# Kernel optimization log

Measured on AMD Instinct MI355X. Metric: run time of the kernel, lower is better.

Reference implementation:

```python
import jax, jax.numpy as jnp
import numpy as np

SUB_NO = 20
T_NO = 200
NB = 19            # cos_basis_no
COS_SHIFT = 1.0
COS_SCALE = 5.0
T_DATA = 100000
E_NO = 2000
I_NO = 400


def _cos_basis():
    x = jnp.arange(T_NO, dtype=jnp.float32)
    raw = COS_SCALE * jnp.log(x + COS_SHIFT)                      # [T_no]
    phi = (jnp.pi / 2.0) * jnp.arange(NB, dtype=jnp.float32)[:, None]  # [NB,1]
    basis = 0.5 * jnp.cos(raw[None, :] - phi) + 0.5               # [NB, T_no]
    mask = (raw[None, :] >= phi - jnp.pi) & (raw[None, :] <= phi + jnp.pi)
    return jnp.where(mask, basis, 0.0)


def _gconv(x, kern_flipped):
    # depthwise (grouped) 1d cross-correlation, VALID padding, matching torch F.conv1d
    # x: [L, sub], kern_flipped: [sub, T_no] (already time-flipped) -> [L - T_no + 1, sub]
    out = jax.lax.conv_general_dilated(
        x.T[None],                      # [1, sub, L]
        kern_flipped[:, None, :],       # [sub, 1, T_no]
        window_strides=(1,), padding='VALID',
        feature_group_count=x.shape[1],
        dimension_numbers=('NCH', 'OIH', 'NCH'))
    return out[0].T


def setup_inputs() -> dict:
    key = jax.random.key(0)
    ks = jax.random.split(key, 16)
    rng = np.random.default_rng(0)
    # tree adjacency: each node j>0 has a parent < j; C_den[parent, child] = 1
    C_den = np.zeros((SUB_NO, SUB_NO), np.float32)
    for j in range(1, SUB_NO):
        C_den[rng.integers(0, j), j] = 1.0
    # one-hot synapse -> subunit maps
    C_syn_e = np.zeros((SUB_NO, E_NO), np.float32)
    C_syn_e[rng.integers(0, SUB_NO, E_NO), np.arange(E_NO)] = 1.0
    C_syn_i = np.zeros((SUB_NO, I_NO), np.float32)
    C_syn_i[rng.integers(0, SUB_NO, I_NO), np.arange(I_NO)] = 1.0
    # sparse binary spike trains
    S_e = (jax.random.uniform(ks[0], (T_DATA, E_NO)) < 0.02).astype(jnp.float32)
    S_i = (jax.random.uniform(ks[1], (T_DATA, I_NO)) < 0.02).astype(jnp.float32)
    Z = (jax.random.uniform(ks[2], (T_DATA, SUB_NO)) < 0.05).astype(jnp.float32)
    return {
        'S_e': S_e, 'S_i': S_i, 'Z': Z,
        'C_den': jnp.asarray(C_den), 'C_syn_e': jnp.asarray(C_syn_e), 'C_syn_i': jnp.asarray(C_syn_i),
        'W_syn': 0.1 * jax.random.normal(ks[3], (SUB_NO, NB, 2)),
        'W_hist': 0.1 * jax.random.normal(ks[4], (SUB_NO, NB)),
        'W_spk': jnp.ones(SUB_NO) + 0.05 * jax.random.normal(ks[5], (SUB_NO,)),
        'Delta_spk': jax.random.uniform(ks[6], (SUB_NO,), maxval=2.0),
        'Tau_spk': 3.0 * jnp.ones(SUB_NO) + 0.1 * jax.random.normal(ks[7], (SUB_NO,)),
        'V_o': jax.random.normal(ks[8], (1,)),
        'Theta': 0.1 * jax.random.normal(ks[9], (SUB_NO,)),
        'weight1': 0.1 * jax.random.normal(ks[10], (SUB_NO, 6)),
        'weight2': 0.1 * jax.random.normal(ks[11], (6, 6)),
        'weight3': 0.1 * jax.random.normal(ks[12], (6, SUB_NO)),
    }


def reference(S_e, S_i, Z, C_den, C_syn_e, C_syn_i, W_syn, W_hist, W_spk,
              Delta_spk, Tau_spk, V_o, Theta, weight1, weight2, weight3):
    cb = _cos_basis()                                  # [NB, T_no]
    sub = C_den.shape[0]
    pad = lambda x, n: jnp.concatenate([jnp.zeros((n, sub), x.dtype), x], axis=0)

    # --- spike_convolve ---
    syn_e = S_e @ C_syn_e.T                            # [T, sub]
    syn_i = S_i @ C_syn_i.T
    e_kern = W_syn[:, :, 0] @ cb                       # [sub, T_no]
    i_kern = W_syn[:, :, 1] @ cb
    filtered_e = _gconv(pad(syn_e, T_NO - 1), jnp.flip(e_kern, 1))
    filtered_i = _gconv(pad(syn_i, T_NO - 1), jnp.flip(i_kern, 1))
    syn = filtered_e + filtered_i                      # [T, sub]

    # --- history and spike kernels (causal, 1-step delayed: pad T_no, drop last) ---
    hist_kern = W_hist @ cb                            # [sub, T_no]
    pad_Z = pad(Z, T_NO)                               # [T + T_no, sub]
    hist_filt = _gconv(pad_Z, jnp.flip(hist_kern, 1))[:-1]   # [T, sub]

    t = jnp.maximum(jnp.arange(T_NO, dtype=jnp.float32)[None, :] - Delta_spk[:, None], 0.0)
    t_tau = t / (Tau_spk[:, None] ** 2)
    spk_kern = t_tau * jnp.exp(-t_tau) * (W_spk[:, None] ** 2)  # [sub, T_no]
    spk_filt = _gconv(pad_Z, jnp.flip(spk_kern, 1))[:-1]        # [T, sub]

    # --- per-subunit loop, vectorized: leaf gather == spk_filt @ C_den.T ---
    sub_in = syn + Theta[None, :] + hist_filt + spk_filt @ C_den.T   # [T, sub]
    h0 = jax.nn.leaky_relu(sub_in)
    h1 = jax.nn.leaky_relu(h0[:, :, None] * weight1[None, :, :])     # [T, sub, 6]
    h2 = jax.nn.leaky_relu(jnp.einsum('tsk,kj->tsj', h1, weight2))   # [T, sub, 6]
    final_Z = jax.nn.sigmoid(jnp.einsum('tsj,js->ts', h2, weight3))  # [T, sub]

    final_V = spk_filt[:, 0] + V_o[0]                  # [T]
    out_filters = jnp.concatenate([e_kern, i_kern, hist_kern, spk_kern], axis=0)  # [4*sub, T_no]
    return final_V, final_Z, out_filters
```

## Files before the change

### kernel.cpp

```cpp
#include <hip/hip_runtime.h>

typedef unsigned short ushort_t;
typedef unsigned int uint_t;

#define T_DATA 100000
#define E_NO 2000
#define I_NO 400
#define SUB 20
#define TNO 200
#define NBASIS 19
#define HEAD 256
#define TAILPAD 2048
#define SIGSTRIDE (HEAD + T_DATA + TAILPAD)
#define TILE 2048
#define RPT 8

#define OFF_Z  ((size_t)T_DATA)
#define OFF_F  ((size_t)T_DATA + (size_t)T_DATA*SUB)

__device__ __forceinline__ float b2f(ushort_t u) {
    union { uint_t i; float f; } v; v.i = ((uint_t)u) << 16; return v.f;
}
__device__ __forceinline__ ushort_t f2b(float f) {
    union { uint_t i; float f_; } v; v.f_ = f;
    uint_t b = v.i;
    uint_t r = (b + 0x7FFFu + ((b >> 16) & 1u)) >> 16;
    return (ushort_t)r;
}
__device__ __forceinline__ float ldin(const void* p, size_t idx, int mode) {
    return mode ? b2f(((const ushort_t*)p)[idx]) : ((const float*)p)[idx];
}
__device__ __forceinline__ void stout(void* p, size_t idx, float val, int mode) {
    if (mode) ((ushort_t*)p)[idx] = f2b(val);
    else      ((float*)p)[idx] = val;
}
__device__ __forceinline__ float f4get(const float4& v, int i) {
    return i == 0 ? v.x : i == 1 ? v.y : i == 2 ? v.z : v.w;
}
__device__ __forceinline__ float pick12(const float4& L, const float4& M, const float4& H, int e) {
    return e < 4 ? f4get(L, e) : e < 8 ? f4get(M, e - 4) : f4get(H, e - 8);
}

__global__ void k_probe(const void* tau, int* flag) {
    if (threadIdx.x == 0) {
        const ushort_t* tu = (const ushort_t*)tau;
        int cnt = 0;
        for (int i = 0; i < 20; ++i) {
            float v = b2f(tu[i]);
            if (v >= 1.5f && v < 6.0f) cnt++;
        }
        *flag = (cnt >= 15) ? 1 : 0;
    }
}

__global__ __launch_bounds__(256) void k0_prep(
        const int* __restrict__ flag,
        const void* Csyn_e, const void* Csyn_i,
        const void* W_syn, const void* W_hist,
        const void* W_spk, const void* Delta, const void* Tau,
        float* ws_f, int* mape, int* mapi, ushort_t* sigs, void* dout) {
    int mode = *flag;
    int bid = blockIdx.x, tid = threadIdx.x;
    if (bid < 80) {
        int kidx = bid / 20, s = bid % 20;
        int tau = tid;
        if (tau < TNO) {
            float val;
            if (kidx < 3) {
                float raw = 5.0f * logf((float)tau + 1.0f);
                val = 0.f;
                for (int b = 0; b < NBASIS; ++b) {
                    float phi = 1.5707963267948966f * (float)b;
                    float d = raw - phi;
                    float basis = (d >= -3.14159265358979f && d <= 3.14159265358979f)
                                  ? (0.5f * cosf(d) + 0.5f) : 0.f;
                    float w = (kidx == 0) ? ldin(W_syn, (size_t)s * NBASIS * 2 + b * 2 + 0, mode)
                            : (kidx == 1) ? ldin(W_syn, (size_t)s * NBASIS * 2 + b * 2 + 1, mode)
                                          : ldin(W_hist, (size_t)s * NBASIS + b, mode);
                    val += w * basis;
                }
            } else {
                float dl = ldin(Delta, s, mode), tu = ldin(Tau, s, mode), wk = ldin(W_spk, s, mode);
                float t = fmaxf((float)tau - dl, 0.f);
                float tt = t / (tu * tu);
                val = tt * expf(-tt) * (wk * wk);
            }
            ws_f[kidx * 4000 + s * TNO + tau] = val;
            stout(dout, OFF_F + (size_t)bid * TNO + tau, val, mode);
        }
    } else if (bid < 96) {
        int e = (bid - 80) * 256 + tid;
        if (e < E_NO) {
            int m = 0;
            for (int s = 0; s < SUB; ++s)
                if (ldin(Csyn_e, (size_t)s * E_NO + e, mode) != 0.f) { m = s; break; }
            mape[e] = m;
        }
    } else if (bid < 98) {
        int e = (bid - 96) * 256 + tid;
        if (e < I_NO) {
            int m = 0;
            for (int s = 0; s < SUB; ++s)
                if (ldin(Csyn_i, (size_t)s * I_NO + e, mode) != 0.f) { m = s; break; }
            mapi[e] = m;
        }
    } else if (bid < 158) {
        int rg = bid - 98;
        int sg = rg / 20, s = rg % 20;
        ushort_t* p = sigs + (size_t)sg * SUB * SIGSTRIDE + (size_t)s * SIGSTRIDE;
        for (int i = tid; i < HEAD; i += 256) p[i] = 0;
        for (int i = tid; i < TAILPAD; i += 256) p[HEAD + T_DATA + i] = 0;
    }
}

__global__ __launch_bounds__(256) void k1_reduce(
        const int* __restrict__ flag,
        const void* __restrict__ S_e, const void* __restrict__ S_i,
        const void* __restrict__ Z,
        const int* __restrict__ mape, const int* __restrict__ mapi,
        ushort_t* __restrict__ sigs) {
    __shared__ int me[E_NO];
    __shared__ int mi[I_NO];
    __shared__ float acc[40];
    int tid = threadIdx.x;
    int mode = *flag;
    for (int i = tid; i < E_NO; i += 256) me[i] = mape[i];
    for (int i = tid; i < I_NO; i += 256) mi[i] = mapi[i];
    ushort_t* syn_e_T = sigs;
    ushort_t* syn_i_T = sigs + (size_t)SUB * SIGSTRIDE;
    ushort_t* z_T     = sigs + (size_t)2 * SUB * SIGSTRIDE;

    for (int row = blockIdx.x; row < T_DATA; row += gridDim.x) {
        if (tid < 40) acc[tid] = 0.f;
        __syncthreads();
        if (tid < 250) {
            float v[8];
            if (mode) {
                uint4 u = *(const uint4*)((const ushort_t*)S_e + (size_t)row * E_NO + tid * 8);
                uint_t wd[4] = {u.x, u.y, u.z, u.w};
                #pragma unroll
                for (int q = 0; q < 4; ++q) {
                    v[2*q]   = b2f((ushort_t)(wd[q] & 0xFFFF));
                    v[2*q+1] = b2f((ushort_t)(wd[q] >> 16));
                }
            } else {
                const float* p = (const float*)S_e + (size_t)row * E_NO + tid * 8;
                float4 a = *(const float4*)p, b = *(const float4*)(p + 4);
                v[0]=a.x; v[1]=a.y; v[2]=a.z; v[3]=a.w;
                v[4]=b.x; v[5]=b.y; v[6]=b.z; v[7]=b.w;
            }
            #pragma unroll
            for (int j = 0; j < 8; ++j)
                if (v[j] != 0.f) atomicAdd(&acc[me[tid * 8 + j]], v[j]);
        }
        if (tid < 50) {
            float v[8];
            if (mode) {
                uint4 u = *(const uint4*)((const ushort_t*)S_i + (size_t)row * I_NO + tid * 8);
                uint_t wd[4] = {u.x, u.y, u.z, u.w};
                #pragma unroll
                for (int q = 0; q < 4; ++q) {
                    v[2*q]   = b2f((ushort_t)(wd[q] & 0xFFFF));
                    v[2*q+1] = b2f((ushort_t)(wd[q] >> 16));
                }
            } else {
                const float* p = (const float*)S_i + (size_t)row * I_NO + tid * 8;
                float4 a = *(const float4*)p, b = *(const float4*)(p + 4);
                v[0]=a.x; v[1]=a.y; v[2]=a.z; v[3]=a.w;
                v[4]=b.x; v[5]=b.y; v[6]=b.z; v[7]=b.w;
            }
            #pragma unroll
            for (int j = 0; j < 8; ++j)
                if (v[j] != 0.f) atomicAdd(&acc[20 + mi[tid * 8 + j]], v[j]);
        }
        if (tid >= 64 && tid < 84) {
            int s = tid - 64;
            float zv = ldin(Z, (size_t)row * SUB + s, mode);
            z_T[(size_t)s * SIGSTRIDE + HEAD + row] = f2b(zv);
        }
        __syncthreads();
        if (tid < 20)      syn_e_T[(size_t)tid * SIGSTRIDE + HEAD + row] = f2b(acc[tid]);
        else if (tid < 40) syn_i_T[(size_t)(tid - 20) * SIGSTRIDE + HEAD + row] = f2b(acc[tid]);
        __syncthreads();
    }
}

__global__ __launch_bounds__(256) void k2_conv(
        const ushort_t* __restrict__ sigs, const float* __restrict__ ws_f,
        ushort_t* __restrict__ base_out, ushort_t* __restrict__ spk_out) {
    __shared__ float X[3 * 2248 + 800];
    float* XE = X;
    float* XI = X + 2248;
    float* ZZ = X + 4496;
    float* KK = X + 6744;
    int s = blockIdx.y;
    int t0 = blockIdx.x * TILE;
    int tid = threadIdx.x;

    for (int k = 0; k < 4; ++k)
        for (int j = tid; j < TNO; j += 256)
            KK[k * TNO + j] = ws_f[k * 4000 + s * TNO + j];

    {
        const ushort_t* g0 = sigs + (size_t)s * SIGSTRIDE + (HEAD - 200) + t0;
        const ushort_t* g1 = g0 + (size_t)SUB * SIGSTRIDE;
        const ushort_t* g2 = g0 + (size_t)2 * SUB * SIGSTRIDE;
        for (int v = tid; v < 281; v += 256) {
            uint4 u = *(const uint4*)(g0 + v * 8);
            float* d = XE + v * 8;
            d[0]=b2f((ushort_t)(u.x&0xFFFF)); d[1]=b2f((ushort_t)(u.x>>16));
            d[2]=b2f((ushort_t)(u.y&0xFFFF)); d[3]=b2f((ushort_t)(u.y>>16));
            d[4]=b2f((ushort_t)(u.z&0xFFFF)); d[5]=b2f((ushort_t)(u.z>>16));
            d[6]=b2f((ushort_t)(u.w&0xFFFF)); d[7]=b2f((ushort_t)(u.w>>16));
        }
        for (int v = tid; v < 281; v += 256) {
            uint4 u = *(const uint4*)(g1 + v * 8);
            float* d = XI + v * 8;
            d[0]=b2f((ushort_t)(u.x&0xFFFF)); d[1]=b2f((ushort_t)(u.x>>16));
            d[2]=b2f((ushort_t)(u.y&0xFFFF)); d[3]=b2f((ushort_t)(u.y>>16));
            d[4]=b2f((ushort_t)(u.z&0xFFFF)); d[5]=b2f((ushort_t)(u.z>>16));
            d[6]=b2f((ushort_t)(u.w&0xFFFF)); d[7]=b2f((ushort_t)(u.w>>16));
        }
        for (int v = tid; v < 281; v += 256) {
            uint4 u = *(const uint4*)(g2 + v * 8);
            float* d = ZZ + v * 8;
            d[0]=b2f((ushort_t)(u.x&0xFFFF)); d[1]=b2f((ushort_t)(u.x>>16));
            d[2]=b2f((ushort_t)(u.y&0xFFFF)); d[3]=b2f((ushort_t)(u.y>>16));
            d[4]=b2f((ushort_t)(u.z&0xFFFF)); d[5]=b2f((ushort_t)(u.z>>16));
            d[6]=b2f((ushort_t)(u.w&0xFFFF)); d[7]=b2f((ushort_t)(u.w>>16));
        }
    }
    __syncthreads();

    float acc[RPT] = {0,0,0,0,0,0,0,0};
    float spk[RPT] = {0,0,0,0,0,0,0,0};
    const float4* XE4 = (const float4*)XE;
    const float4* XI4 = (const float4*)XI;
    const float4* ZZ4 = (const float4*)ZZ;
    const float4* KE4 = (const float4*)(KK);
    const float4* KI4 = (const float4*)(KK + 200);
    const float4* KH4 = (const float4*)(KK + 400);
    const float4* KS4 = (const float4*)(KK + 600);
    int w4 = 2 * tid + 49;
    float4 eL = XE4[w4], eM = XE4[w4 + 1], eH = XE4[w4 + 2];
    float4 iL = XI4[w4], iM = XI4[w4 + 1], iH = XI4[w4 + 2];
    float4 zL = ZZ4[w4], zM = ZZ4[w4 + 1], zH = ZZ4[w4 + 2];

    for (int c = 0; c < 50; ++c) {
        if (c > 0) {
            eH = eM; eM = eL; eL = XE4[w4 - c];
            iH = iM; iM = iL; iL = XI4[w4 - c];
            zH = zM; zM = zL; zL = ZZ4[w4 - c];
        }
        float4 ke = KE4[c], ki = KI4[c], kh = KH4[c], ks = KS4[c];
        #pragma unroll
        for (int u = 0; u < 4; ++u) {
            float keu = f4get(ke, u), kiu = f4get(ki, u);
            float khu = f4get(kh, u), ksu = f4get(ks, u);
            #pragma unroll
            for (int r = 0; r < RPT; ++r) {
                float xe = pick12(eL, eM, eH, 4 + r - u);
                float xi = pick12(iL, iM, iH, 4 + r - u);
                float zz = pick12(zL, zM, zH, 3 + r - u);
                acc[r] += keu * xe;
                acc[r] += kiu * xi;
                acc[r] += khu * zz;
                spk[r] += ksu * zz;
            }
        }
    }
    int tbase = t0 + RPT * tid;
    if (tbase + RPT <= T_DATA) {
        uint4 pb, pq;
        pb.x = (uint_t)f2b(acc[0]) | ((uint_t)f2b(acc[1]) << 16);
        pb.y = (uint_t)f2b(acc[2]) | ((uint_t)f2b(acc[3]) << 16);
        pb.z = (uint_t)f2b(acc[4]) | ((uint_t)f2b(acc[5]) << 16);
        pb.w = (uint_t)f2b(acc[6]) | ((uint_t)f2b(acc[7]) << 16);
        pq.x = (uint_t)f2b(spk[0]) | ((uint_t)f2b(spk[1]) << 16);
        pq.y = (uint_t)f2b(spk[2]) | ((uint_t)f2b(spk[3]) << 16);
        pq.z = (uint_t)f2b(spk[4]) | ((uint_t)f2b(spk[5]) << 16);
        pq.w = (uint_t)f2b(spk[6]) | ((uint_t)f2b(spk[7]) << 16);
        *(uint4*)(base_out + (size_t)s * T_DATA + tbase) = pb;
        *(uint4*)(spk_out + (size_t)s * T_DATA + tbase) = pq;
    } else {
        #pragma unroll
        for (int r = 0; r < RPT; ++r) {
            int t = tbase + r;
            if (t < T_DATA) {
                base_out[(size_t)s * T_DATA + t] = f2b(acc[r]);
                spk_out[(size_t)s * T_DATA + t] = f2b(spk[r]);
            }
        }
    }
}

__global__ __launch_bounds__(256) void k3_mlp(
        const int* __restrict__ flag,
        const ushort_t* __restrict__ base_out, const ushort_t* __restrict__ spk_out,
        const void* __restrict__ C_den, const void* __restrict__ Theta,
        const void* __restrict__ Vo,
        const void* __restrict__ w1, const void* __restrict__ w2,
        const void* __restrict__ w3,
        void* __restrict__ dout) {
    __shared__ float cd[400], th[20], W1[120], W2[36], W3[120];
    __shared__ float vo;
    int tid = threadIdx.x;
    int mode = *flag;
    for (int i = tid; i < 400; i += 256) cd[i] = ldin(C_den, i, mode);
    if (tid < 20) th[tid] = ldin(Theta, tid, mode);
    if (tid < 120) W1[tid] = ldin(w1, tid, mode);
    if (tid < 36) W2[tid] = ldin(w2, tid, mode);
    if (tid >= 128 && tid < 248) W3[tid - 128] = ldin(w3, tid - 128, mode);
    if (tid == 0) vo = ldin(Vo, 0, mode);
    __syncthreads();
    int t = blockIdx.x * 256 + tid;
    if (t >= T_DATA) return;
    float sv[20], bv[20];
    #pragma unroll
    for (int c = 0; c < 20; ++c) {
        sv[c] = b2f(spk_out[(size_t)c * T_DATA + t]);
        bv[c] = b2f(base_out[(size_t)c * T_DATA + t]);
    }
    stout(dout, (size_t)t, sv[0] + vo, mode);
    #pragma unroll
    for (int p = 0; p < 20; ++p) {
        float ps = 0.f;
        #pragma unroll
        for (int c = 0; c < 20; ++c) ps += cd[p * 20 + c] * sv[c];
        float x = bv[p] + th[p] + ps;
        float h0 = x >= 0.f ? x : 0.01f * x;
        float h1[6];
        #pragma unroll
        for (int k = 0; k < 6; ++k) {
            float y = h0 * W1[p * 6 + k];
            h1[k] = y >= 0.f ? y : 0.01f * y;
        }
        float zacc = 0.f;
        #pragma unroll
        for (int j = 0; j < 6; ++j) {
            float a = 0.f;
            #pragma unroll
            for (int k = 0; k < 6; ++k) a += h1[k] * W2[k * 6 + j];
            float h2 = a >= 0.f ? a : 0.01f * a;
            zacc += h2 * W3[j * 20 + p];
        }
        float zv = 1.f / (1.f + expf(-zacc));
        stout(dout, OFF_Z + (size_t)t * SUB + p, zv, mode);
    }
}

extern "C" void kernel_launch(void* const* d_in, const int* in_sizes, int n_in,
                              void* d_out, int out_size, void* d_ws, size_t ws_size,
                              hipStream_t stream) {
    const void* S_e     = d_in[0];
    const void* S_i     = d_in[1];
    const void* Z       = d_in[2];
    const void* C_den   = d_in[3];
    const void* C_syn_e = d_in[4];
    const void* C_syn_i = d_in[5];
    const void* W_syn   = d_in[6];
    const void* W_hist  = d_in[7];
    const void* W_spk   = d_in[8];
    const void* Delta   = d_in[9];
    const void* Tau     = d_in[10];
    const void* Vo      = d_in[11];
    const void* Theta   = d_in[12];
    const void* w1      = d_in[13];
    const void* w2      = d_in[14];
    const void* w3      = d_in[15];

    char* w = (char*)d_ws;
    int*      flag     = (int*)w;
    float*    ws_f     = (float*)(w + 64);
    int*      mape     = (int*)(w + 64 + 64000);
    int*      mapi     = (int*)(w + 64 + 64000 + 8000);
    ushort_t* sigs     = (ushort_t*)(w + 73664);
    ushort_t* base_out = (ushort_t*)(w + 12350144);
    ushort_t* spk_out  = (ushort_t*)(w + 16350144);

    hipLaunchKernelGGL(k_probe, dim3(1), dim3(64), 0, stream, Tau, flag);
    hipLaunchKernelGGL(k0_prep, dim3(158), dim3(256), 0, stream,
                       flag, C_syn_e, C_syn_i, W_syn, W_hist, W_spk, Delta, Tau,
                       ws_f, mape, mapi, sigs, d_out);
    hipLaunchKernelGGL(k1_reduce, dim3(2048), dim3(256), 0, stream,
                       flag, S_e, S_i, Z, mape, mapi, sigs);
    hipLaunchKernelGGL(k2_conv, dim3((T_DATA + TILE - 1) / TILE, SUB), dim3(256), 0, stream,
                       sigs, ws_f, base_out, spk_out);
    hipLaunchKernelGGL(k3_mlp, dim3((T_DATA + 255) / 256), dim3(256), 0, stream,
                       flag, base_out, spk_out, C_den, Theta, Vo, w1, w2, w3, d_out);
}
```

Baseline: 314.1 us.

## Reduce spike rows per wave into shared tile and write transposed signals coalesced

The synapse reduction kernel now gives each block a span of 128 time rows, with each wavefront handling one row per iteration. Per-row accumulators live in a shared [60 x 132] tile, so there are no block-wide barriers per row. Z values are staged in the same tile, and at the end the tile is written out as packed 4-element bf16 chunks along time instead of scattered 2-byte stores. This removes per-row __syncthreads and uncoalesced transposed writes, at the cost of a larger shared footprint and smaller blocks processing more serial work.

```diff
diff --git a/kernel.cpp b/kernel.cpp
--- a/kernel.cpp
+++ b/kernel.cpp
@@ -14,6 +14,8 @@
 #define SIGSTRIDE (HEAD + T_DATA + TAILPAD)
 #define TILE 2048
 #define RPT 8
+#define TSPAN 128
+#define SLOTSTR 132
 
 #define OFF_Z  ((size_t)T_DATA)
 #define OFF_F  ((size_t)T_DATA + (size_t)T_DATA*SUB)
@@ -121,67 +123,91 @@
         ushort_t* __restrict__ sigs) {
     __shared__ int me[E_NO];
     __shared__ int mi[I_NO];
-    __shared__ float acc[40];
+    __shared__ float acc[60 * SLOTSTR];
     int tid = threadIdx.x;
     int mode = *flag;
+    int wave = tid >> 6, lane = tid & 63;
     for (int i = tid; i < E_NO; i += 256) me[i] = mape[i];
     for (int i = tid; i < I_NO; i += 256) mi[i] = mapi[i];
-    ushort_t* syn_e_T = sigs;
-    ushort_t* syn_i_T = sigs + (size_t)SUB * SIGSTRIDE;
-    ushort_t* z_T     = sigs + (size_t)2 * SUB * SIGSTRIDE;
-
-    for (int row = blockIdx.x; row < T_DATA; row += gridDim.x) {
-        if (tid < 40) acc[tid] = 0.f;
-        __syncthreads();
-        if (tid < 250) {
-            float v[8];
-            if (mode) {
-                uint4 u = *(const uint4*)((const ushort_t*)S_e + (size_t)row * E_NO + tid * 8);
+    for (int i = tid; i < 60 * SLOTSTR; i += 256) acc[i] = 0.f;
+    __syncthreads();
+
+    int base = blockIdx.x * TSPAN;
+    for (int it = 0; it < TSPAN / 4; ++it) {
+        int rl = it * 4 + wave;
+        int row = base + rl;
+        if (row >= T_DATA) continue;
+        if (mode) {
+            const ushort_t* pe = (const ushort_t*)S_e + (size_t)row * E_NO;
+            #pragma unroll
+            for (int rd = 0; rd < 4; ++rd) {
+                int idx = rd * 64 + lane;
+                if (idx < 250) {
+                    uint4 u = *(const uint4*)(pe + idx * 8);
+                    uint_t wd[4] = {u.x, u.y, u.z, u.w};
+                    #pragma unroll
+                    for (int q = 0; q < 4; ++q) {
+                        float a = b2f((ushort_t)(wd[q] & 0xFFFF));
+                        float b = b2f((ushort_t)(wd[q] >> 16));
+                        if (a != 0.f) atomicAdd(&acc[me[idx * 8 + 2 * q] * SLOTSTR + rl], a);
+                        if (b != 0.f) atomicAdd(&acc[me[idx * 8 + 2 * q + 1] * SLOTSTR + rl], b);
+                    }
+                }
+            }
+            const ushort_t* pi = (const ushort_t*)S_i + (size_t)row * I_NO;
+            if (lane < 50) {
+                uint4 u = *(const uint4*)(pi + lane * 8);
                 uint_t wd[4] = {u.x, u.y, u.z, u.w};
                 #pragma unroll
                 for (int q = 0; q < 4; ++q) {
-                    v[2*q]   = b2f((ushort_t)(wd[q] & 0xFFFF));
-                    v[2*q+1] = b2f((ushort_t)(wd[q] >> 16));
+                    float a = b2f((ushort_t)(wd[q] & 0xFFFF));
+                    float b = b2f((ushort_t)(wd[q] >> 16));
+                    if (a != 0.f) atomicAdd(&acc[(20 + mi[lane * 8 + 2 * q]) * SLOTSTR + rl], a);
+                    if (b != 0.f) atomicAdd(&acc[(20 + mi[lane * 8 + 2 * q + 1]) * SLOTSTR + rl], b);
                 }
-            } else {
-                const float* p = (const float*)S_e + (size_t)row * E_NO + tid * 8;
-                float4 a = *(const float4*)p, b = *(const float4*)(p + 4);
-                v[0]=a.x; v[1]=a.y; v[2]=a.z; v[3]=a.w;
-                v[4]=b.x; v[5]=b.y; v[6]=b.z; v[7]=b.w;
-            }
+            }
+        } else {
+            const float* pe = (const float*)S_e + (size_t)row * E_NO;
             #pragma unroll
-            for (int j = 0; j < 8; ++j)
-                if (v[j] != 0.f) atomicAdd(&acc[me[tid * 8 + j]], v[j]);
-        }
-        if (tid < 50) {
-            float v[8];
-            if (mode) {
-                uint4 u = *(const uint4*)((const ushort_t*)S_i + (size_t)row * I_NO + tid * 8);
-                uint_t wd[4] = {u.x, u.y, u.z, u.w};
-                #pragma unroll
-                for (int q = 0; q < 4; ++q) {
-                    v[2*q]   = b2f((ushort_t)(wd[q] & 0xFFFF));
-                    v[2*q+1] = b2f((ushort_t)(wd[q] >> 16));
+            for (int rd = 0; rd < 8; ++rd) {
+                int idx = rd * 64 + lane;
+                if (idx < 500) {
+                    float4 u = *(const float4*)(pe + idx * 4);
+                    float v[4] = {u.x, u.y, u.z, u.w};
+                    #pragma unroll
+                    for (int q = 0; q < 4; ++q)
+                        if (v[q] != 0.f) atomicAdd(&acc[me[idx * 4 + q] * SLOTSTR + rl], v[q]);
                 }
-            } else {
-                const float* p = (const float*)S_i + (size_t)row * I_NO + tid * 8;
-                float4 a = *(const float4*)p, b = *(const float4*)(p + 4);
-                v[0]=a.x; v[1]=a.y; v[2]=a.z; v[3]=a.w;
-                v[4]=b.x; v[5]=b.y; v[6]=b.z; v[7]=b.w;
-            }
+            }
+            const float* pi = (const float*)S_i + (size_t)row * I_NO;
             #pragma unroll
-            for (int j = 0; j < 8; ++j)
-                if (v[j] != 0.f) atomicAdd(&acc[20 + mi[tid * 8 + j]], v[j]);
-        }
-        if (tid >= 64 && tid < 84) {
-            int s = tid - 64;
-            float zv = ldin(Z, (size_t)row * SUB + s, mode);
-            z_T[(size_t)s * SIGSTRIDE + HEAD + row] = f2b(zv);
-        }
-        __syncthreads();
-        if (tid < 20)      syn_e_T[(size_t)tid * SIGSTRIDE + HEAD + row] = f2b(acc[tid]);
-        else if (tid < 40) syn_i_T[(size_t)(tid - 20) * SIGSTRIDE + HEAD + row] = f2b(acc[tid]);
-        __syncthreads();
+            for (int rd = 0; rd < 2; ++rd) {
+                int idx = rd * 64 + lane;
+                if (idx < 100) {
+                    float4 u = *(const float4*)(pi + idx * 4);
+                    float v[4] = {u.x, u.y, u.z, u.w};
+                    #pragma unroll
+                    for (int q = 0; q < 4; ++q)
+                        if (v[q] != 0.f) atomicAdd(&acc[(20 + mi[idx * 4 + q]) * SLOTSTR + rl], v[q]);
+                }
+            }
+        }
+        if (lane < 20)
+            acc[(40 + lane) * SLOTSTR + rl] = ldin(Z, (size_t)row * SUB + lane, mode);
+    }
+    __syncthreads();
+
+    for (int idx = tid; idx < 60 * (TSPAN / 4); idx += 256) {
+        int sig = idx >> 5;
+        int g = idx & 31;
+        int t0 = g * 4;
+        if (base + t0 >= T_DATA) continue;
+        const float* src = &acc[sig * SLOTSTR + t0];
+        float4 v = *(const float4*)src;
+        uint2 o;
+        o.x = (uint_t)f2b(v.x) | ((uint_t)f2b(v.y) << 16);
+        o.y = (uint_t)f2b(v.z) | ((uint_t)f2b(v.w) << 16);
+        *(uint2*)(sigs + (size_t)sig * SIGSTRIDE + HEAD + base + t0) = o;
     }
 }
 
@@ -382,7 +408,7 @@
     hipLaunchKernelGGL(k0_prep, dim3(158), dim3(256), 0, stream,
                        flag, C_syn_e, C_syn_i, W_syn, W_hist, W_spk, Delta, Tau,
                        ws_f, mape, mapi, sigs, d_out);
-    hipLaunchKernelGGL(k1_reduce, dim3(2048), dim3(256), 0, stream,
+    hipLaunchKernelGGL(k1_reduce, dim3((T_DATA + TSPAN - 1) / TSPAN), dim3(256), 0, stream,
                        flag, S_e, S_i, Z, mape, mapi, sigs);
     hipLaunchKernelGGL(k2_conv, dim3((T_DATA + TILE - 1) / TILE, SUB), dim3(256), 0, stream,
                        sigs, ws_f, base_out, spk_out);
```

Result: slower. 564.4 us (+79.7%).
